# Performance work log

Hardware: AMD Instinct MI355X
Metric: run time of the kernel (lower is better)

The kernel has to match this reference:

```python
import jax, jax.numpy as jnp
import numpy as np

N, E, G = 50000, 800000, 16
H, C = 4, 64  # heads, per-head channels
NEG_SLOPE = 0.2

def gat_conv(x, src, dst, W, att_s, att_d, bias, heads, out_c, concat):
    # x: [N, Fin]; W: [Fin, heads*out_c]; att_s/att_d: [heads, out_c]
    h = (x @ W).reshape(N, heads, out_c)
    a_s = (h * att_s).sum(-1)              # [N, heads]
    a_d = (h * att_d).sum(-1)
    e = a_s[src] + a_d[dst]                # [E, heads]
    e = jnp.where(e >= 0, e, NEG_SLOPE * e)  # leaky_relu
    m = jax.ops.segment_max(e, dst, num_segments=N)
    ex = jnp.exp(e - m[dst])
    den = jax.ops.segment_sum(ex, dst, num_segments=N)
    alpha = ex / (den[dst] + 1e-16)        # segment softmax over incoming edges
    msg = h[src] * alpha[:, :, None]       # [E, heads, out_c]
    out = jax.ops.segment_sum(msg, dst, num_segments=N)
    out = out.reshape(N, heads * out_c) if concat else out.mean(axis=1)
    return out + bias

def setup_inputs() -> dict:
    key = jax.random.key(0)
    ks = jax.random.split(key, 30)
    def g(k, shape, scale=0.05):
        return (jax.random.normal(k, shape, dtype=jnp.float32) * scale)
    inp = {}
    inp['x'] = jax.random.normal(ks[0], (N, 32), dtype=jnp.float32)
    inp['edge_index'] = jax.random.randint(ks[1], (2, E), 0, N, dtype=jnp.int32)
    inp['batch'] = jnp.sort(jax.random.randint(ks[2], (N,), 0, G, dtype=jnp.int32))
    inp['global_features'] = jax.random.normal(ks[3], (G, 4), dtype=jnp.float32)
    # node encoder
    inp['W_enc'] = g(ks[4], (32, C)); inp['b_enc'] = g(ks[5], (C,))
    # conv1: 64 -> 4x64 concat
    inp['W1'] = g(ks[6], (C, H * C)); inp['as1'] = g(ks[7], (H, C)); inp['ad1'] = g(ks[8], (H, C)); inp['b1'] = g(ks[9], (H * C,))
    # conv2: 256 -> 4x64 concat
    inp['W2'] = g(ks[10], (H * C, H * C)); inp['as2'] = g(ks[11], (H, C)); inp['ad2'] = g(ks[12], (H, C)); inp['b2'] = g(ks[13], (H * C,))
    # conv3: 256 -> 1x64 no concat
    inp['W3'] = g(ks[14], (H * C, C)); inp['as3'] = g(ks[15], (1, C)); inp['ad3'] = g(ks[16], (1, C)); inp['b3'] = g(ks[17], (C,))
    # global processor
    inp['Wg'] = g(ks[18], (4, C)); inp['bg'] = g(ks[19], (C,))
    # decoder
    inp['Wd1'] = g(ks[20], (2 * C, C)); inp['bd1'] = g(ks[21], (C,))
    inp['gamma'] = jnp.ones((C,), jnp.float32); inp['beta'] = jnp.zeros((C,), jnp.float32)
    inp['Wd2'] = g(ks[22], (C, 256)); inp['bd2'] = g(ks[23], (256,))
    return inp

def reference(x, edge_index, batch, global_features, W_enc, b_enc,
              W1, as1, ad1, b1, W2, as2, ad2, b2, W3, as3, ad3, b3,
              Wg, bg, Wd1, bd1, gamma, beta, Wd2, bd2):
    # add self-loops (PyG GATConv default)
    loops = jnp.arange(N, dtype=edge_index.dtype)
    src = jnp.concatenate([edge_index[0], loops])
    dst = jnp.concatenate([edge_index[1], loops])
    h = x @ W_enc + b_enc
    h = gat_conv(h, src, dst, W1, as1, ad1, b1, H, C, True)
    h = jax.nn.elu(h)  # dropout is identity in eval
    h = gat_conv(h, src, dst, W2, as2, ad2, b2, H, C, True)
    h = jax.nn.elu(h)
    h = gat_conv(h, src, dst, W3, as3, ad3, b3, 1, C, False)
    # global mean pool per graph
    sums = jax.ops.segment_sum(h, batch, num_segments=G)
    cnts = jax.ops.segment_sum(jnp.ones((N, 1), h.dtype), batch, num_segments=G)
    pooled = sums / jnp.maximum(cnts, 1.0)
    genc = jax.nn.relu(global_features @ Wg + bg)
    z = jnp.concatenate([pooled, genc], axis=1)
    z = z @ Wd1 + bd1
    z = z * gamma + beta  # BatchNorm1d in eval mode (running stats 0/1)
    z = jax.nn.relu(z)
    out = z @ Wd2 + bd2
    return jax.nn.softmax(out, axis=1)
```

## Files before the change

kernel.cpp:

```cpp
#include <hip/hip_runtime.h>
#include <math.h>

#define NEG_SLOPE 0.2f
#define LOG2E 1.4426950408889634f

typedef __attribute__((ext_vector_type(8))) short short8;
typedef __attribute__((ext_vector_type(4))) float f32x4;

__device__ inline float b2f_lo(unsigned int u) {
    union { unsigned int i; float f; } x; x.i = u << 16; return x.f;
}
__device__ inline float b2f_hi(unsigned int u) {
    union { unsigned int i; float f; } x; x.i = u & 0xFFFF0000u; return x.f;
}
__device__ inline unsigned short f2b(float f) {
    union { float f; unsigned int i; } u; u.f = f;
    unsigned int r = u.i + 0x7FFF + ((u.i >> 16) & 1);
    return (unsigned short)(r >> 16);
}

__global__ void prep_kernel(const float* __restrict__ W_enc, const float* __restrict__ b_enc,
                            const float* __restrict__ W1, const float* __restrict__ W2,
                            const float* __restrict__ W3, const float* __restrict__ as1,
                            const float* __restrict__ ad1, const float* __restrict__ b1,
                            unsigned short* __restrict__ Wc1t, float* __restrict__ bc1,
                            unsigned short* __restrict__ Wt2, unsigned short* __restrict__ Wt3,
                            float* __restrict__ u1s, float* __restrict__ u1d,
                            int* __restrict__ counts, float* __restrict__ pooledP,
                            float* __restrict__ cntP, int N, int G, int zc) {
    const int b = blockIdx.x;
    const int t = threadIdx.x;
    if (b < 32) {
        int i = b * 256 + t;
        int h = i >> 11, rem = i & 2047, o = rem >> 5, j = rem & 31;
        float s = 0.0f;
        for (int k = 0; k < 64; k++)
            s += W_enc[j * 64 + k] * W1[k * 256 + h * 64 + o];
        Wc1t[i] = f2b(s);
    } else if (b == 32) {
        float s = b1[t];
        for (int k = 0; k < 64; k++) s += b_enc[k] * W1[k * 256 + t];
        bc1[t] = s;
    } else if (b == 33) {
        int k = t >> 2, h = t & 3;
        float s = 0.0f, d = 0.0f;
        for (int c = 0; c < 64; c++) {
            float w = W1[k * 256 + h * 64 + c];
            s += w * as1[h * 64 + c];
            d += w * ad1[h * 64 + c];
        }
        u1s[k * 4 + h] = s;
        u1d[k * 4 + h] = d;
    } else if (b < 34 + 256) {
        int i = (b - 34) * 256 + t;
        int k = i >> 8, m = i & 255;
        Wt2[(size_t)m * 256 + k] = f2b(W2[i]);
    } else if (b < 34 + 256 + 64) {
        int i = (b - 290) * 256 + t;
        int k = i >> 6, m = i & 63;
        Wt3[(size_t)m * 256 + k] = f2b(W3[i]);
    } else if (b < 354 + zc) {
        int i = (b - 354) * 256 + t;
        if (i < N) counts[i] = 0;
    } else {
        int i = (b - 354 - zc) * 256 + t;
        if (i < 64 * G * 64) pooledP[i] = 0.0f;
        if (i < 64 * G) cntP[i] = 0.0f;
    }
}

__global__ __launch_bounds__(256) void score_x(
        const float* __restrict__ x, const float* __restrict__ W_enc,
        const float* __restrict__ b_enc,
        const float* __restrict__ u1s, const float* __restrict__ u1d,
        unsigned short* __restrict__ x16, float* __restrict__ a_s,
        float* __restrict__ a_d, int N) {
    __shared__ float sUs[32][4], sUd[32][4], sC[8];
    __shared__ float sX[32][33];
    const int t = threadIdx.x;
    if (t < 128) {
        int j = t >> 2, h = t & 3;
        float s = 0.0f, d = 0.0f;
        for (int k = 0; k < 64; k++) {
            float w = W_enc[j * 64 + k];
            s += w * u1s[k * 4 + h];
            d += w * u1d[k * 4 + h];
        }
        sUs[j][h] = s; sUd[j][h] = d;
    } else if (t < 136) {
        int hh = t - 128;
        const float* u = (hh < 4) ? u1s : u1d;
        int h = hh & 3;
        float c = 0.0f;
        for (int k = 0; k < 64; k++) c += b_enc[k] * u[k * 4 + h];
        sC[hh] = c;
    }
    const int n0 = blockIdx.x * 32;
    const int row = t >> 3, col = (t & 7) << 2;
    float4 xv = {0, 0, 0, 0};
    if (n0 + row < N) xv = *(const float4*)&x[(size_t)(n0 + row) * 32 + col];
    sX[row][col + 0] = xv.x; sX[row][col + 1] = xv.y;
    sX[row][col + 2] = xv.z; sX[row][col + 3] = xv.w;
    __syncthreads();
    const int ni = t >> 3, oi = t & 7, h = oi & 3;
    const bool isS = oi < 4;
    float acc = sC[oi];
    #pragma unroll 8
    for (int j = 0; j < 32; j++) acc += sX[ni][j] * (isS ? sUs[j][h] : sUd[j][h]);
    if (n0 + ni < N) {
        float* out = isS ? a_s : a_d;
        out[(size_t)(n0 + ni) * 4 + h] = acc * LOG2E;
    }
    if (n0 + row < N) {
        ushort4 o = {f2b(xv.x), f2b(xv.y), f2b(xv.z), f2b(xv.w)};
        *(ushort4*)&x16[(size_t)(n0 + row) * 32 + col] = o;
    }
}

template<int CPW, int SCORES>
__global__ __launch_bounds__(256) void gemm_mfma(const unsigned short* __restrict__ A16,
                                                 const unsigned short* __restrict__ Bt16,
                                                 unsigned short* __restrict__ C16,
                                                 const float* __restrict__ att_s,
                                                 const float* __restrict__ att_d,
                                                 float* __restrict__ a_s,
                                                 float* __restrict__ a_d,
                                                 int Nrows, int K, int M, int H) {
    constexpr int BN = CPW * 64;
    __shared__ unsigned short sA[64][40];
    __shared__ unsigned short sB[BN][40];
    const int tid = threadIdx.x;
    const int wave = tid >> 6;
    const int lane = tid & 63;
    const int quad = lane >> 4;
    const int l16 = lane & 15;
    const int row0 = blockIdx.x * 64;
    const int col0 = blockIdx.y * BN;
    const int sr = tid >> 2;
    const int sk = (tid & 3) << 3;

    f32x4 acc[4][CPW];
    #pragma unroll
    for (int i = 0; i < 4; i++)
        #pragma unroll
        for (int j = 0; j < CPW; j++) acc[i][j] = (f32x4){0,0,0,0};

    for (int kt = 0; kt < K; kt += 32) {
        __syncthreads();
        {
            int r = row0 + sr;
            uint4 z = {0,0,0,0};
            *(uint4*)&sA[sr][sk] = (r < Nrows) ? *(const uint4*)&A16[(size_t)r * K + kt + sk] : z;
        }
        #pragma unroll
        for (int i = 0; i < CPW; i++) {
            int c = col0 + sr + i * 64;
            *(uint4*)&sB[sr + i * 64][sk] = *(const uint4*)&Bt16[(size_t)c * K + kt + sk];
        }
        __syncthreads();
        short8 bf[CPW];
        #pragma unroll
        for (int j = 0; j < CPW; j++)
            bf[j] = *(const short8*)&sB[wave * (CPW * 16) + j * 16 + l16][quad * 8];
        #pragma unroll
        for (int i = 0; i < 4; i++) {
            short8 af = *(const short8*)&sA[i * 16 + l16][quad * 8];
            #pragma unroll
            for (int j = 0; j < CPW; j++)
                acc[i][j] = __builtin_amdgcn_mfma_f32_16x16x32_bf16(af, bf[j], acc[i][j], 0, 0, 0);
        }
    }
    if (SCORES) {
        __shared__ float sSD[64][CPW][2];
        for (int t = tid; t < 64 * CPW * 2; t += 256) ((float*)sSD)[t] = 0.0f;
        __syncthreads();
        const int hib = (wave * CPW * 16) >> 6;
        float avs[CPW], avd[CPW];
        #pragma unroll
        for (int j = 0; j < CPW; j++) {
            int c = col0 + wave * (CPW * 16) + j * 16 + l16;
            avs[j] = att_s[c];
            avd[j] = att_d[c];
        }
        #pragma unroll
        for (int i = 0; i < 4; i++) {
            float ps[4] = {0,0,0,0}, pd[4] = {0,0,0,0};
            #pragma unroll
            for (int j = 0; j < CPW; j++)
                #pragma unroll
                for (int r = 0; r < 4; r++) {
                    ps[r] += acc[i][j][r] * avs[j];
                    pd[r] += acc[i][j][r] * avd[j];
                }
            #pragma unroll
            for (int off = 1; off < 16; off <<= 1)
                #pragma unroll
                for (int r = 0; r < 4; r++) {
                    ps[r] += __shfl_xor(ps[r], off);
                    pd[r] += __shfl_xor(pd[r], off);
                }
            if (l16 == 0) {
                #pragma unroll
                for (int r = 0; r < 4; r++) {
                    atomicAdd(&sSD[i * 16 + quad * 4 + r][hib][0], ps[r]);
                    atomicAdd(&sSD[i * 16 + quad * 4 + r][hib][1], pd[r]);
                }
            }
        }
        __syncthreads();
        for (int t = tid; t < 64 * CPW; t += 256) {
            int row = t & 63, hb = t >> 6;
            int r = row0 + row;
            if (r < Nrows) {
                int hg = (col0 >> 6) + hb;
                a_s[r * H + hg] = sSD[row][hb][0] * LOG2E;
                a_d[r * H + hg] = sSD[row][hb][1] * LOG2E;
            }
        }
    }
    #pragma unroll
    for (int i = 0; i < 4; i++) {
        #pragma unroll
        for (int j = 0; j < CPW; j++) {
            int col = col0 + wave * (CPW * 16) + j * 16 + l16;
            #pragma unroll
            for (int r = 0; r < 4; r++) {
                int row = row0 + i * 16 + quad * 4 + r;
                if (row < Nrows) C16[(size_t)row * M + col] = f2b(acc[i][j][r]);
            }
        }
    }
}

__global__ __launch_bounds__(256) void gemm_bd32(const unsigned short* __restrict__ A16,
                                                 const unsigned short* __restrict__ Bt16,
                                                 const float* __restrict__ bias,
                                                 unsigned short* __restrict__ C16,
                                                 int Nrows) {
    __shared__ unsigned short sA[64][40];
    __shared__ unsigned short sB[64][40];
    const int tid = threadIdx.x;
    const int wave = tid >> 6;
    const int lane = tid & 63;
    const int quad = lane >> 4;
    const int l16 = lane & 15;
    const int h = blockIdx.y;
    const int row0 = blockIdx.x * 64;
    const int sr = tid >> 2;
    const int sk = (tid & 3) << 3;

    {
        int r = row0 + sr;
        uint4 z = {0,0,0,0};
        *(uint4*)&sA[sr][sk] = (r < Nrows)
            ? *(const uint4*)&A16[(size_t)r * 128 + h * 32 + sk] : z;
        *(uint4*)&sB[sr][sk] = *(const uint4*)&Bt16[(size_t)(h * 64 + sr) * 32 + sk];
    }
    __syncthreads();
    short8 bf = *(const short8*)&sB[wave * 16 + l16][quad * 8];
    f32x4 acc[4];
    #pragma unroll
    for (int i = 0; i < 4; i++) {
        short8 af = *(const short8*)&sA[i * 16 + l16][quad * 8];
        acc[i] = __builtin_amdgcn_mfma_f32_16x16x32_bf16(af, bf, (f32x4){0,0,0,0}, 0, 0, 0);
    }
    const int col = h * 64 + wave * 16 + l16;
    const float bb = bias[col];
    #pragma unroll
    for (int i = 0; i < 4; i++) {
        #pragma unroll
        for (int r = 0; r < 4; r++) {
            int row = row0 + i * 16 + quad * 4 + r;
            if (row < Nrows) {
                float v = acc[i][r] + bb;
                v = (v > 0.0f) ? v : expm1f(v);
                C16[(size_t)row * 256 + col] = f2b(v);
            }
        }
    }
}

__global__ void edge_hist_kernel(const int* __restrict__ ei, int* __restrict__ counts,
                                 int E, int Et) {
    int e = blockIdx.x * 256 + threadIdx.x;
    if (e >= Et) return;
    int d = (e < E) ? ei[E + e] : e - E;
    atomicAdd(&counts[d], 1);
}

__global__ __launch_bounds__(1024) void scan_blocks(int* __restrict__ counts,
                                                    int* __restrict__ blockSums, int N) {
    __shared__ int wsum[16];
    const int tid = threadIdx.x;
    const int lane = tid & 63;
    const int wave = tid >> 6;
    int i = blockIdx.x * 1024 + tid;
    int v = (i < N) ? counts[i] : 0;
    int s = v;
    #pragma unroll
    for (int off = 1; off < 64; off <<= 1) {
        int t = __shfl_up(s, off);
        if (lane >= off) s += t;
    }
    if (lane == 63) wsum[wave] = s;
    __syncthreads();
    if (wave == 0 && lane < 16) {
        int ws = wsum[lane];
        #pragma unroll
        for (int off = 1; off < 16; off <<= 1) {
            int t = __shfl_up(ws, off);
            if (lane >= off) ws += t;
        }
        wsum[lane] = ws;
    }
    __syncthreads();
    int waveOff = (wave > 0) ? wsum[wave - 1] : 0;
    int incl = s + waveOff;
    if (i < N) counts[i] = incl - v;
    if (tid == 1023) blockSums[blockIdx.x] = incl;
}

__global__ void scan_add2(const int* __restrict__ excl, const int* __restrict__ blockSums,
                          int nb, int* __restrict__ offsets, int* __restrict__ cursor,
                          int N, int Et) {
    __shared__ int sbs[64];
    if (threadIdx.x < 64) {
        int lane = threadIdx.x;
        int v = (lane < nb) ? blockSums[lane] : 0;
        int s = v;
        #pragma unroll
        for (int off = 1; off < 64; off <<= 1) {
            int t = __shfl_up(s, off);
            if (lane >= off) s += t;
        }
        sbs[lane] = s - v;
    }
    __syncthreads();
    int i = blockIdx.x * 256 + threadIdx.x;
    if (i < N) {
        int o = excl[i] + sbs[i >> 10];
        offsets[i] = o;
        cursor[i] = o;
    }
    if (i == N) offsets[N] = Et;
}

__global__ void edge_sort_kernel(const int* __restrict__ ei, int* __restrict__ cursor,
                                 int* __restrict__ srcS, int E, int Et) {
    int e = blockIdx.x * 256 + threadIdx.x;
    if (e >= Et) return;
    int s, d;
    if (e < E) { s = ei[e]; d = ei[E + e]; } else { s = d = e - E; }
    int pos = atomicAdd(&cursor[d], 1);
    srcS[pos] = s;
}

__global__ __launch_bounds__(256) void gat_agg_x32(
        const int* __restrict__ offsets, const int* __restrict__ srcS,
        const float4* __restrict__ a_s4, const float4* __restrict__ a_d4,
        const unsigned short* __restrict__ x16,
        unsigned short* __restrict__ aggX,
        int N) {
    __shared__ float4 wlds[4][64];
    __shared__ int slds[4][64];
    const int wid = threadIdx.x >> 6;
    const int n = blockIdx.x * 4 + wid;
    if (n >= N) return;
    const int lane = threadIdx.x & 63;
    const int q = lane >> 4;
    const int l16 = lane & 15;
    const int start = offsets[n], end = offsets[n + 1];
    const float4 ad = a_d4[n];
    float2 acc0 = {0,0}, acc1 = {0,0}, acc2 = {0,0}, acc3 = {0,0};
    float4 den = {0,0,0,0};
    const int loff = l16 << 1;

    for (int e0 = start; e0 < end; e0 += 64) {
        const int cnt = min(64, end - e0);
        if (lane < cnt) {
            int sB = srcS[e0 + lane];
            slds[wid][lane] = sB;
            const float4 as = a_s4[sB];
            float x0 = as.x + ad.x; x0 = fmaxf(x0, NEG_SLOPE * x0);
            float x1 = as.y + ad.y; x1 = fmaxf(x1, NEG_SLOPE * x1);
            float x2 = as.z + ad.z; x2 = fmaxf(x2, NEG_SLOPE * x2);
            float x3 = as.w + ad.w; x3 = fmaxf(x3, NEG_SLOPE * x3);
            wlds[wid][lane] = (float4){exp2f(x0), exp2f(x1), exp2f(x2), exp2f(x3)};
        }
        int j = q;
        for (; j + 12 < cnt; j += 16) {
            int ss[4]; float4 ww[4]; unsigned int gg[4];
            #pragma unroll
            for (int u = 0; u < 4; u++) {
                ss[u] = slds[wid][j + 4 * u];
                ww[u] = wlds[wid][j + 4 * u];
            }
            #pragma unroll
            for (int u = 0; u < 4; u++)
                gg[u] = *(const unsigned int*)&x16[((size_t)ss[u] << 5) + loff];
            #pragma unroll
            for (int u = 0; u < 4; u++) {
                const float vl = b2f_lo(gg[u]), vh = b2f_hi(gg[u]);
                acc0.x += ww[u].x * vl; acc0.y += ww[u].x * vh;
                acc1.x += ww[u].y * vl; acc1.y += ww[u].y * vh;
                acc2.x += ww[u].z * vl; acc2.y += ww[u].z * vh;
                acc3.x += ww[u].w * vl; acc3.y += ww[u].w * vh;
                den.x += ww[u].x; den.y += ww[u].y; den.z += ww[u].z; den.w += ww[u].w;
            }
        }
        for (; j + 4 < cnt; j += 8) {
            const int s0 = slds[wid][j], s1 = slds[wid][j + 4];
            const float4 w0 = wlds[wid][j], w1 = wlds[wid][j + 4];
            const unsigned int g0 = *(const unsigned int*)&x16[((size_t)s0 << 5) + loff];
            const unsigned int g1 = *(const unsigned int*)&x16[((size_t)s1 << 5) + loff];
            const float vl0 = b2f_lo(g0), vh0 = b2f_hi(g0);
            const float vl1 = b2f_lo(g1), vh1 = b2f_hi(g1);
            acc0.x += w0.x * vl0 + w1.x * vl1; acc0.y += w0.x * vh0 + w1.x * vh1;
            acc1.x += w0.y * vl0 + w1.y * vl1; acc1.y += w0.y * vh0 + w1.y * vh1;
            acc2.x += w0.z * vl0 + w1.z * vl1; acc2.y += w0.z * vh0 + w1.z * vh1;
            acc3.x += w0.w * vl0 + w1.w * vl1; acc3.y += w0.w * vh0 + w1.w * vh1;
            den.x += w0.x + w1.x; den.y += w0.y + w1.y;
            den.z += w0.z + w1.z; den.w += w0.w + w1.w;
        }
        for (; j < cnt; j += 4) {
            const int s = slds[wid][j];
            const float4 w = wlds[wid][j];
            const unsigned int g = *(const unsigned int*)&x16[((size_t)s << 5) + loff];
            const float vl = b2f_lo(g), vh = b2f_hi(g);
            acc0.x += w.x * vl; acc0.y += w.x * vh;
            acc1.x += w.y * vl; acc1.y += w.y * vh;
            acc2.x += w.z * vl; acc2.y += w.z * vh;
            acc3.x += w.w * vl; acc3.y += w.w * vh;
            den.x += w.x; den.y += w.y; den.z += w.z; den.w += w.w;
        }
    }
    #pragma unroll
    for (int off = 16; off < 64; off <<= 1) {
        acc0.x += __shfl_xor(acc0.x, off); acc0.y += __shfl_xor(acc0.y, off);
        acc1.x += __shfl_xor(acc1.x, off); acc1.y += __shfl_xor(acc1.y, off);
        acc2.x += __shfl_xor(acc2.x, off); acc2.y += __shfl_xor(acc2.y, off);
        acc3.x += __shfl_xor(acc3.x, off); acc3.y += __shfl_xor(acc3.y, off);
        den.x += __shfl_xor(den.x, off); den.y += __shfl_xor(den.y, off);
        den.z += __shfl_xor(den.z, off); den.w += __shfl_xor(den.w, off);
    }
    if (q == 0) {
        const float i0 = 1.0f / (den.x + 1e-16f);
        const float i1 = 1.0f / (den.y + 1e-16f);
        const float i2 = 1.0f / (den.z + 1e-16f);
        const float i3 = 1.0f / (den.w + 1e-16f);
        unsigned int o0 = (unsigned int)f2b(acc0.x * i0) | ((unsigned int)f2b(acc0.y * i0) << 16);
        unsigned int o1 = (unsigned int)f2b(acc1.x * i1) | ((unsigned int)f2b(acc1.y * i1) << 16);
        unsigned int o2 = (unsigned int)f2b(acc2.x * i2) | ((unsigned int)f2b(acc2.y * i2) << 16);
        unsigned int o3 = (unsigned int)f2b(acc3.x * i3) | ((unsigned int)f2b(acc3.y * i3) << 16);
        *(unsigned int*)&aggX[((size_t)n << 7) + 0 * 32 + loff] = o0;
        *(unsigned int*)&aggX[((size_t)n << 7) + 1 * 32 + loff] = o1;
        *(unsigned int*)&aggX[((size_t)n << 7) + 2 * 32 + loff] = o2;
        *(unsigned int*)&aggX[((size_t)n << 7) + 3 * 32 + loff] = o3;
    }
}

__global__ __launch_bounds__(256) void gat_fused4(
        const int* __restrict__ offsets, const int* __restrict__ srcS,
        const float4* __restrict__ a_s4, const float4* __restrict__ a_d4,
        const unsigned short* __restrict__ hW16, const float* __restrict__ bias,
        unsigned short* __restrict__ out16, int N) {
    __shared__ float wlds[4][64][4];
    __shared__ int slds[4][64];
    const int wid = threadIdx.x >> 6;
    const int n = blockIdx.x * 4 + wid;
    if (n >= N) return;
    const int lane = threadIdx.x & 63;
    const int quad = lane >> 4;
    const int start = offsets[n], end = offsets[n + 1];
    const float4 ad = a_d4[n];
    float4 acc = {0, 0, 0, 0};
    float den = 0.0f;
    const int loff = lane << 2;

    for (int e0 = start; e0 < end; e0 += 64) {
        const int cnt = min(64, end - e0);
        if (lane < cnt) {
            int sB = srcS[e0 + lane];
            slds[wid][lane] = sB;
            const float4 as = a_s4[sB];
            float x0 = as.x + ad.x; x0 = fmaxf(x0, NEG_SLOPE * x0);
            float x1 = as.y + ad.y; x1 = fmaxf(x1, NEG_SLOPE * x1);
            float x2 = as.z + ad.z; x2 = fmaxf(x2, NEG_SLOPE * x2);
            float x3 = as.w + ad.w; x3 = fmaxf(x3, NEG_SLOPE * x3);
            wlds[wid][lane][0] = exp2f(x0);
            wlds[wid][lane][1] = exp2f(x1);
            wlds[wid][lane][2] = exp2f(x2);
            wlds[wid][lane][3] = exp2f(x3);
        }
        int j = 0;
        for (; j + 4 <= cnt; j += 4) {
            const int s0 = __builtin_amdgcn_readfirstlane(slds[wid][j + 0]);
            const int s1 = __builtin_amdgcn_readfirstlane(slds[wid][j + 1]);
            const int s2 = __builtin_amdgcn_readfirstlane(slds[wid][j + 2]);
            const int s3 = __builtin_amdgcn_readfirstlane(slds[wid][j + 3]);
            const float w0 = wlds[wid][j + 0][quad];
            const float w1 = wlds[wid][j + 1][quad];
            const float w2 = wlds[wid][j + 2][quad];
            const float w3 = wlds[wid][j + 3][quad];
            const uint2 h0 = *(const uint2*)&hW16[((size_t)s0 << 8) + loff];
            const uint2 h1 = *(const uint2*)&hW16[((size_t)s1 << 8) + loff];
            const uint2 h2 = *(const uint2*)&hW16[((size_t)s2 << 8) + loff];
            const uint2 h3 = *(const uint2*)&hW16[((size_t)s3 << 8) + loff];
            acc.x += w0 * b2f_lo(h0.x); acc.y += w0 * b2f_hi(h0.x);
            acc.z += w0 * b2f_lo(h0.y); acc.w += w0 * b2f_hi(h0.y);
            acc.x += w1 * b2f_lo(h1.x); acc.y += w1 * b2f_hi(h1.x);
            acc.z += w1 * b2f_lo(h1.y); acc.w += w1 * b2f_hi(h1.y);
            acc.x += w2 * b2f_lo(h2.x); acc.y += w2 * b2f_hi(h2.x);
            acc.z += w2 * b2f_lo(h2.y); acc.w += w2 * b2f_hi(h2.y);
            acc.x += w3 * b2f_lo(h3.x); acc.y += w3 * b2f_hi(h3.x);
            acc.z += w3 * b2f_lo(h3.y); acc.w += w3 * b2f_hi(h3.y);
            den += (w0 + w1) + (w2 + w3);
        }
        for (; j < cnt; j++) {
            const int s = __builtin_amdgcn_readfirstlane(slds[wid][j]);
            const float w = wlds[wid][j][quad];
            const uint2 hv = *(const uint2*)&hW16[((size_t)s << 8) + loff];
            acc.x += w * b2f_lo(hv.x); acc.y += w * b2f_hi(hv.x);
            acc.z += w * b2f_lo(hv.y); acc.w += w * b2f_hi(hv.y);
            den += w;
        }
    }

    const float inv = 1.0f / (den + 1e-16f);
    const float4 bb = *(const float4*)&bias[loff];
    float v0 = acc.x * inv + bb.x; v0 = (v0 > 0.0f) ? v0 : expm1f(v0);
    float v1 = acc.y * inv + bb.y; v1 = (v1 > 0.0f) ? v1 : expm1f(v1);
    float v2 = acc.z * inv + bb.z; v2 = (v2 > 0.0f) ? v2 : expm1f(v2);
    float v3 = acc.w * inv + bb.w; v3 = (v3 > 0.0f) ? v3 : expm1f(v3);
    uint2 o;
    o.x = (unsigned int)f2b(v0) | ((unsigned int)f2b(v1) << 16);
    o.y = (unsigned int)f2b(v2) | ((unsigned int)f2b(v3) << 16);
    *(uint2*)&out16[(size_t)n * 256 + loff] = o;
}

__global__ __launch_bounds__(256) void gat_fused1(
        const int* __restrict__ offsets, const int* __restrict__ srcS,
        const float* __restrict__ a_s, const float* __restrict__ a_d,
        const unsigned short* __restrict__ hW16, const float* __restrict__ bias,
        const int* __restrict__ batch,
        float* __restrict__ pooledP, float* __restrict__ cntP, int N, int G) {
    __shared__ float wlds[4][64];
    __shared__ int slds[4][64];
    __shared__ float2 sOut[4][32];
    __shared__ int sG[4];
    const int wid = threadIdx.x >> 6;
    const int n = blockIdx.x * 4 + wid;
    const bool valid = n < N;
    const int lane = threadIdx.x & 63;
    const int half = lane >> 5;
    const int l32 = lane & 31;
    const int start = valid ? offsets[n] : 0;
    const int end   = valid ? offsets[n + 1] : 0;
    const float ad  = valid ? a_d[n] : 0.0f;
    float accx = 0.0f, accy = 0.0f, den = 0.0f;
    const int loff = l32 << 1;

    for (int e0 = start; e0 < end; e0 += 64) {
        const int cnt_ = min(64, end - e0);
        if (lane < cnt_) {
            int sB = srcS[e0 + lane];
            slds[wid][lane] = sB;
            float ev = a_s[sB] + ad;
            ev = fmaxf(ev, NEG_SLOPE * ev);
            wlds[wid][lane] = exp2f(ev);
        }
        int j = half;
        for (; j + 8 <= cnt_ + half; j += 8) {
            const int s0 = slds[wid][j + 0];
            const int s1 = slds[wid][j + 2];
            const int s2 = slds[wid][j + 4];
            const int s3 = slds[wid][j + 6];
            const float w0 = wlds[wid][j + 0];
            const float w1 = wlds[wid][j + 2];
            const float w2 = wlds[wid][j + 4];
            const float w3 = wlds[wid][j + 6];
            const unsigned int h0 = *(const unsigned int*)&hW16[((size_t)s0 << 6) + loff];
            const unsigned int h1 = *(const unsigned int*)&hW16[((size_t)s1 << 6) + loff];
            const unsigned int h2 = *(const unsigned int*)&hW16[((size_t)s2 << 6) + loff];
            const unsigned int h3 = *(const unsigned int*)&hW16[((size_t)s3 << 6) + loff];
            accx += w0 * b2f_lo(h0); accy += w0 * b2f_hi(h0);
            accx += w1 * b2f_lo(h1); accy += w1 * b2f_hi(h1);
            accx += w2 * b2f_lo(h2); accy += w2 * b2f_hi(h2);
            accx += w3 * b2f_lo(h3); accy += w3 * b2f_hi(h3);
            den += (w0 + w1) + (w2 + w3);
        }
        for (; j < cnt_; j += 2) {
            const int s = slds[wid][j];
            const float w = wlds[wid][j];
            const unsigned int hv = *(const unsigned int*)&hW16[((size_t)s << 6) + loff];
            accx += w * b2f_lo(hv);
            accy += w * b2f_hi(hv);
            den += w;
        }
    }
    accx += __shfl_xor(accx, 32);
    accy += __shfl_xor(accy, 32);
    den  += __shfl_xor(den, 32);
    if (half == 0) {
        if (valid) {
            const float inv = 1.0f / (den + 1e-16f);
            sOut[wid][l32] = (float2){accx * inv + bias[loff], accy * inv + bias[loff + 1]};
        } else {
            sOut[wid][l32] = (float2){0.0f, 0.0f};
        }
        if (l32 == 0) sG[wid] = valid ? batch[n] : -1;
    }
    __syncthreads();
    const int p = blockIdx.x & 63;
    if (wid == 0 && half == 0) {
        const int g0 = sG[0], g1 = sG[1], g2 = sG[2], g3 = sG[3];
        if (g0 >= 0 && g1 == g0 && g2 == g0 && g3 == g0) {
            const float2 s0 = sOut[0][l32], s1 = sOut[1][l32];
            const float2 s2 = sOut[2][l32], s3 = sOut[3][l32];
            float* base = pooledP + ((size_t)p * G + g0) * 64;
            atomicAdd(&base[loff],     (s0.x + s1.x) + (s2.x + s3.x));
            atomicAdd(&base[loff + 1], (s0.y + s1.y) + (s2.y + s3.y));
            if (l32 == 0) atomicAdd(&cntP[p * G + g0], 4.0f);
        } else {
            #pragma unroll
            for (int w = 0; w < 4; w++) {
                const int g = sG[w];
                if (g >= 0) {
                    const float2 s = sOut[w][l32];
                    float* base = pooledP + ((size_t)p * G + g) * 64;
                    atomicAdd(&base[loff], s.x);
                    atomicAdd(&base[loff + 1], s.y);
                    if (l32 == 0) atomicAdd(&cntP[p * G + g], 1.0f);
                }
            }
        }
    }
}

__global__ __launch_bounds__(256) void final_kernel(
        const float* __restrict__ pooledP, const float* __restrict__ cntP,
        const float* __restrict__ gf, const float* __restrict__ Wg,
        const float* __restrict__ bg, const float* __restrict__ Wd1,
        const float* __restrict__ bd1, const float* __restrict__ gamma,
        const float* __restrict__ beta, const float* __restrict__ Wd2,
        const float* __restrict__ bd2, float* __restrict__ out, int G) {
    const int g = blockIdx.x;
    const int tid = threadIdx.x;
    const int lane = tid & 63;
    const int wave = tid >> 6;
    __shared__ float sPart[4][64];
    __shared__ float sCntTot;
    __shared__ float spg[128];
    __shared__ float sz[64];
    __shared__ float wred[8];

    {
        const int c = lane;
        const int pg = wave;
        float a = 0.0f;
        #pragma unroll
        for (int p = 0; p < 16; p++)
            a += pooledP[((size_t)(pg * 16 + p) * G + g) * 64 + c];
        sPart[pg][c] = a;
        if (pg == 1) {
            float cv = cntP[c * G + g];
            #pragma unroll
            for (int off = 32; off > 0; off >>= 1) cv += __shfl_xor(cv, off);
            if (c == 0) sCntTot = cv;
        }
    }
    __syncthreads();
    if (tid < 64) {
        spg[tid] = (sPart[0][tid] + sPart[1][tid] + sPart[2][tid] + sPart[3][tid])
                   / fmaxf(sCntTot, 1.0f);
    } else if (tid < 128) {
        int c = tid - 64;
        float v = bg[c];
        #pragma unroll
        for (int k = 0; k < 4; k++) v += gf[g * 4 + k] * Wg[k * 64 + c];
        spg[64 + c] = fmaxf(v, 0.0f);
    }
    __syncthreads();
    if (tid < 64) {
        float v = bd1[tid];
        #pragma unroll 8
        for (int k = 0; k < 128; k++) v += spg[k] * Wd1[k * 64 + tid];
        v = v * gamma[tid] + beta[tid];
        sz[tid] = fmaxf(v, 0.0f);
    }
    __syncthreads();
    float v = bd2[tid];
    #pragma unroll 8
    for (int k = 0; k < 64; k++) v += sz[k] * Wd2[k * 256 + tid];
    float m = v;
    #pragma unroll
    for (int off = 32; off > 0; off >>= 1) m = fmaxf(m, __shfl_xor(m, off));
    if (lane == 0) wred[wave] = m;
    __syncthreads();
    float M = fmaxf(fmaxf(wred[0], wred[1]), fmaxf(wred[2], wred[3]));
    float e = expf(v - M);
    float s = e;
    #pragma unroll
    for (int off = 32; off > 0; off >>= 1) s += __shfl_xor(s, off);
    if (lane == 0) wred[4 + wave] = s;
    __syncthreads();
    float S = (wred[4] + wred[5]) + (wred[6] + wred[7]);
    out[g * 256 + tid] = e / S;
}

extern "C" void kernel_launch(void* const* d_in, const int* in_sizes, int n_in,
                              void* d_out, int out_size, void* d_ws, size_t ws_size,
                              hipStream_t stream) {
    const float* x     = (const float*)d_in[0];
    const int*   ei    = (const int*)  d_in[1];
    const int*   batch = (const int*)  d_in[2];
    const float* gf    = (const float*)d_in[3];
    const float* W_enc = (const float*)d_in[4];
    const float* b_enc = (const float*)d_in[5];
    const float* W1  = (const float*)d_in[6];
    const float* as1 = (const float*)d_in[7];
    const float* ad1 = (const float*)d_in[8];
    const float* b1  = (const float*)d_in[9];
    const float* W2  = (const float*)d_in[10];
    const float* as2 = (const float*)d_in[11];
    const float* ad2 = (const float*)d_in[12];
    const float* b2  = (const float*)d_in[13];
    const float* W3  = (const float*)d_in[14];
    const float* as3 = (const float*)d_in[15];
    const float* ad3 = (const float*)d_in[16];
    const float* b3  = (const float*)d_in[17];
    const float* Wg  = (const float*)d_in[18];
    const float* bg  = (const float*)d_in[19];
    const float* Wd1 = (const float*)d_in[20];
    const float* bd1 = (const float*)d_in[21];
    const float* gm  = (const float*)d_in[22];
    const float* bt  = (const float*)d_in[23];
    const float* Wd2 = (const float*)d_in[24];
    const float* bd2 = (const float*)d_in[25];

    const int N  = in_sizes[2];
    const int E  = in_sizes[1] / 2;
    const int G  = in_sizes[3] / 4;
    const int Et = E + N;

    unsigned short* h16a = (unsigned short*)d_ws;
    unsigned short* h16b = h16a + (size_t)N * 256;
    unsigned short* h1_16 = h16b + (size_t)N * 256;
    unsigned short* x16  = h1_16 + (size_t)N * 64;
    unsigned short* Wc1t = x16 + (size_t)N * 32;
    unsigned short* Wt2  = Wc1t + 4 * 64 * 32;
    unsigned short* Wt3  = Wt2 + 256 * 256;
    float* bc1    = (float*)(Wt3 + 64 * 256);
    float* a_s    = bc1 + 256;
    float* a_d    = a_s + (size_t)N * 4;
    float* u1s    = a_d + (size_t)N * 4;
    float* u1d    = u1s + 256;
    float* pooledP = u1d + 256;
    float* cntP   = pooledP + (size_t)64 * G * 64;
    int*   offsets = (int*)(cntP + 64 * G);
    int*   srcS    = offsets + (N + 1);
    int*   counts  = srcS + Et;
    int*   cursor  = counts + N;
    int*   blockSums = cursor + N;

    dim3 blk(256);
    auto cdiv = [](int a, int b) { return (a + b - 1) / b; };
    const int eBlocks = cdiv(Et, 256);
    const int rowBlocks = cdiv(N, 64);
    const int nScanBlocks = cdiv(N, 1024);
    const int zc = cdiv(N, 256);
    const int z2 = cdiv(64 * G * 64, 256);

    prep_kernel<<<354 + zc + z2, blk, 0, stream>>>(W_enc, b_enc, W1, W2, W3, as1, ad1, b1,
                                                   Wc1t, bc1, Wt2, Wt3, u1s, u1d,
                                                   counts, pooledP, cntP, N, G, zc);
    edge_hist_kernel<<<eBlocks, blk, 0, stream>>>(ei, counts, E, Et);
    scan_blocks<<<nScanBlocks, 1024, 0, stream>>>(counts, blockSums, N);
    scan_add2<<<cdiv(N + 1, 256), blk, 0, stream>>>(counts, blockSums, nScanBlocks,
                                                    offsets, cursor, N, Et);
    edge_sort_kernel<<<eBlocks, blk, 0, stream>>>(ei, cursor, srcS, E, Et);

    score_x<<<cdiv(N, 32), blk, 0, stream>>>(x, W_enc, b_enc, u1s, u1d, x16, a_s, a_d, N);

    gat_agg_x32<<<cdiv(N, 4), blk, 0, stream>>>(offsets, srcS, (const float4*)a_s,
                                                (const float4*)a_d, x16, h16a, N);
    gemm_bd32<<<dim3(rowBlocks, 4), blk, 0, stream>>>(h16a, Wc1t, bc1, h16b, N);

    gemm_mfma<2, 1><<<dim3(rowBlocks, 2), blk, 0, stream>>>(h16b, Wt2, h16a,
                                                            as2, ad2, a_s, a_d, N, 256, 256, 4);
    gat_fused4<<<cdiv(N, 4), blk, 0, stream>>>(offsets, srcS, (const float4*)a_s,
                                               (const float4*)a_d, h16a, b2, h16b, N);

    gemm_mfma<1, 1><<<dim3(rowBlocks, 1), blk, 0, stream>>>(h16b, Wt3, h1_16,
                                                            as3, ad3, a_s, a_d, N, 256, 64, 1);
    gat_fused1<<<cdiv(N, 4), blk, 0, stream>>>(offsets, srcS, a_s, a_d, h1_16, b3,
                                               batch, pooledP, cntP, N, G);

    final_kernel<<<G, blk, 0, stream>>>(pooledP, cntP, gf, Wg, bg, Wd1, bd1, gm, bt, Wd2, bd2,
                                        (float*)d_out, G);
}
```

Measured before the change: 424.6 us.

## Fuse conv1 output GEMM into conv2 GEMM and precompute conv3 attention scores

Merges the per-head conv1 projection (bias plus ELU) with the conv2 weight GEMM into one kernel. The 64x256 intermediate tile now stays in LDS and is never written to or reread from global memory. Conv3 attention logits are computed inside gat_fused4 by dotting the ELU output with W3·att vectors precomputed in prep, so the conv3 GEMM drops its score epilogue. In exchange the fused kernel uses about 54KB of LDS and launches one block per row tile instead of 2D grids, which lowers occupancy and parallelism. The conv3 scores come from fp32 activations rather than the bf16-rounded GEMM output, so they differ slightly numerically.

```diff
diff --git a/kernel.cpp b/kernel.cpp
--- a/kernel.cpp
+++ b/kernel.cpp
@@ -23,9 +23,11 @@
                             const float* __restrict__ W1, const float* __restrict__ W2,
                             const float* __restrict__ W3, const float* __restrict__ as1,
                             const float* __restrict__ ad1, const float* __restrict__ b1,
+                            const float* __restrict__ as3, const float* __restrict__ ad3,
                             unsigned short* __restrict__ Wc1t, float* __restrict__ bc1,
                             unsigned short* __restrict__ Wt2, unsigned short* __restrict__ Wt3,
                             float* __restrict__ u1s, float* __restrict__ u1d,
+                            float* __restrict__ u3s, float* __restrict__ u3d,
                             int* __restrict__ counts, float* __restrict__ pooledP,
                             float* __restrict__ cntP, int N, int G, int zc) {
     const int b = blockIdx.x;
@@ -51,19 +53,27 @@
         }
         u1s[k * 4 + h] = s;
         u1d[k * 4 + h] = d;
-    } else if (b < 34 + 256) {
-        int i = (b - 34) * 256 + t;
+    } else if (b == 34) {
+        float s = 0.0f, d = 0.0f;
+        for (int o = 0; o < 64; o++) {
+            float w = W3[t * 64 + o];
+            s += w * as3[o];
+            d += w * ad3[o];
+        }
+        u3s[t] = s; u3d[t] = d;
+    } else if (b < 35 + 256) {
+        int i = (b - 35) * 256 + t;
         int k = i >> 8, m = i & 255;
         Wt2[(size_t)m * 256 + k] = f2b(W2[i]);
-    } else if (b < 34 + 256 + 64) {
-        int i = (b - 290) * 256 + t;
+    } else if (b < 35 + 256 + 64) {
+        int i = (b - 291) * 256 + t;
         int k = i >> 6, m = i & 63;
         Wt3[(size_t)m * 256 + k] = f2b(W3[i]);
-    } else if (b < 354 + zc) {
-        int i = (b - 354) * 256 + t;
+    } else if (b < 355 + zc) {
+        int i = (b - 355) * 256 + t;
         if (i < N) counts[i] = 0;
     } else {
-        int i = (b - 354 - zc) * 256 + t;
+        int i = (b - 355 - zc) * 256 + t;
         if (i < 64 * G * 64) pooledP[i] = 0.0f;
         if (i < 64 * G) cntP[i] = 0.0f;
     }
@@ -232,49 +242,136 @@
     }
 }
 
-__global__ __launch_bounds__(256) void gemm_bd32(const unsigned short* __restrict__ A16,
-                                                 const unsigned short* __restrict__ Bt16,
-                                                 const float* __restrict__ bias,
-                                                 unsigned short* __restrict__ C16,
-                                                 int Nrows) {
-    __shared__ unsigned short sA[64][40];
-    __shared__ unsigned short sB[64][40];
+__global__ __launch_bounds__(256) void gemm_c12(
+        const unsigned short* __restrict__ aggX,
+        const unsigned short* __restrict__ Wc1t,
+        const float* __restrict__ bc1,
+        const unsigned short* __restrict__ Wt2,
+        const float* __restrict__ att_s,
+        const float* __restrict__ att_d,
+        float* __restrict__ a_s, float* __restrict__ a_d,
+        unsigned short* __restrict__ C16,
+        int Nrows) {
+    __shared__ unsigned short sH[64][264];
+    __shared__ unsigned short sB[256][40];
+    __shared__ float sSD[64][4][2];
     const int tid = threadIdx.x;
     const int wave = tid >> 6;
     const int lane = tid & 63;
     const int quad = lane >> 4;
     const int l16 = lane & 15;
-    const int h = blockIdx.y;
     const int row0 = blockIdx.x * 64;
     const int sr = tid >> 2;
     const int sk = (tid & 3) << 3;
 
+    #pragma unroll
+    for (int h = 0; h < 4; h++) {
+        __syncthreads();
+        {
+            int r = row0 + sr;
+            uint4 z = {0,0,0,0};
+            *(uint4*)&sB[sr][sk] = (r < Nrows)
+                ? *(const uint4*)&aggX[(size_t)r * 128 + h * 32 + sk] : z;
+            *(uint4*)&sB[64 + sr][sk] = *(const uint4*)&Wc1t[(size_t)(h * 64 + sr) * 32 + sk];
+        }
+        __syncthreads();
+        short8 bf = *(const short8*)&sB[64 + wave * 16 + l16][quad * 8];
+        const int col = h * 64 + wave * 16 + l16;
+        const float bb = bc1[col];
+        #pragma unroll
+        for (int i = 0; i < 4; i++) {
+            short8 af = *(const short8*)&sB[i * 16 + l16][quad * 8];
+            f32x4 acc = __builtin_amdgcn_mfma_f32_16x16x32_bf16(af, bf, (f32x4){0,0,0,0}, 0, 0, 0);
+            #pragma unroll
+            for (int r = 0; r < 4; r++) {
+                float v = acc[r] + bb;
+                v = (v > 0.0f) ? v : expm1f(v);
+                sH[i * 16 + quad * 4 + r][col] = f2b(v);
+            }
+        }
+    }
+
+    f32x4 acc2[4][4];
+    #pragma unroll
+    for (int i = 0; i < 4; i++)
+        #pragma unroll
+        for (int j = 0; j < 4; j++) acc2[i][j] = (f32x4){0,0,0,0};
+
+    for (int kt = 0; kt < 256; kt += 32) {
+        __syncthreads();
+        #pragma unroll
+        for (int i = 0; i < 4; i++) {
+            int c = sr + i * 64;
+            *(uint4*)&sB[c][sk] = *(const uint4*)&Wt2[(size_t)c * 256 + kt + sk];
+        }
+        __syncthreads();
+        short8 bf2[4];
+        #pragma unroll
+        for (int j = 0; j < 4; j++)
+            bf2[j] = *(const short8*)&sB[wave * 64 + j * 16 + l16][quad * 8];
+        #pragma unroll
+        for (int i = 0; i < 4; i++) {
+            short8 af = *(const short8*)&sH[i * 16 + l16][kt + quad * 8];
+            #pragma unroll
+            for (int j = 0; j < 4; j++)
+                acc2[i][j] = __builtin_amdgcn_mfma_f32_16x16x32_bf16(af, bf2[j], acc2[i][j], 0, 0, 0);
+        }
+    }
+
     {
-        int r = row0 + sr;
-        uint4 z = {0,0,0,0};
-        *(uint4*)&sA[sr][sk] = (r < Nrows)
-            ? *(const uint4*)&A16[(size_t)r * 128 + h * 32 + sk] : z;
-        *(uint4*)&sB[sr][sk] = *(const uint4*)&Bt16[(size_t)(h * 64 + sr) * 32 + sk];
-    }
-    __syncthreads();
-    short8 bf = *(const short8*)&sB[wave * 16 + l16][quad * 8];
-    f32x4 acc[4];
+        for (int t = tid; t < 512; t += 256) ((float*)sSD)[t] = 0.0f;
+        __syncthreads();
+        float avs[4], avd[4];
+        #pragma unroll
+        for (int j = 0; j < 4; j++) {
+            int c = wave * 64 + j * 16 + l16;
+            avs[j] = att_s[c];
+            avd[j] = att_d[c];
+        }
+        #pragma unroll
+        for (int i = 0; i < 4; i++) {
+            float ps[4] = {0,0,0,0}, pd[4] = {0,0,0,0};
+            #pragma unroll
+            for (int j = 0; j < 4; j++)
+                #pragma unroll
+                for (int r = 0; r < 4; r++) {
+                    ps[r] += acc2[i][j][r] * avs[j];
+                    pd[r] += acc2[i][j][r] * avd[j];
+                }
+            #pragma unroll
+            for (int off = 1; off < 16; off <<= 1)
+                #pragma unroll
+                for (int r = 0; r < 4; r++) {
+                    ps[r] += __shfl_xor(ps[r], off);
+                    pd[r] += __shfl_xor(pd[r], off);
+                }
+            if (l16 == 0) {
+                #pragma unroll
+                for (int r = 0; r < 4; r++) {
+                    atomicAdd(&sSD[i * 16 + quad * 4 + r][wave][0], ps[r]);
+                    atomicAdd(&sSD[i * 16 + quad * 4 + r][wave][1], pd[r]);
+                }
+            }
+        }
+        __syncthreads();
+        {
+            int row = tid & 63, hb = tid >> 6;
+            int r = row0 + row;
+            if (r < Nrows) {
+                a_s[r * 4 + hb] = sSD[row][hb][0] * LOG2E;
+                a_d[r * 4 + hb] = sSD[row][hb][1] * LOG2E;
+            }
+        }
+    }
     #pragma unroll
     for (int i = 0; i < 4; i++) {
-        short8 af = *(const short8*)&sA[i * 16 + l16][quad * 8];
-        acc[i] = __builtin_amdgcn_mfma_f32_16x16x32_bf16(af, bf, (f32x4){0,0,0,0}, 0, 0, 0);
-    }
-    const int col = h * 64 + wave * 16 + l16;
-    const float bb = bias[col];
-    #pragma unroll
-    for (int i = 0; i < 4; i++) {
-        #pragma unroll
-        for (int r = 0; r < 4; r++) {
-            int row = row0 + i * 16 + quad * 4 + r;
-            if (row < Nrows) {
-                float v = acc[i][r] + bb;
-                v = (v > 0.0f) ? v : expm1f(v);
-                C16[(size_t)row * 256 + col] = f2b(v);
+        #pragma unroll
+        for (int j = 0; j < 4; j++) {
+            int col = wave * 64 + j * 16 + l16;
+            #pragma unroll
+            for (int r = 0; r < 4; r++) {
+                int row = row0 + i * 16 + quad * 4 + r;
+                if (row < Nrows) C16[(size_t)row * 256 + col] = f2b(acc2[i][j][r]);
             }
         }
     }
@@ -463,6 +560,8 @@
         const int* __restrict__ offsets, const int* __restrict__ srcS,
         const float4* __restrict__ a_s4, const float4* __restrict__ a_d4,
         const unsigned short* __restrict__ hW16, const float* __restrict__ bias,
+        const float* __restrict__ u3s, const float* __restrict__ u3d,
+        float* __restrict__ a_s3, float* __restrict__ a_d3,
         unsigned short* __restrict__ out16, int N) {
     __shared__ float wlds[4][64][4];
     __shared__ int slds[4][64];
@@ -532,6 +631,21 @@
     float v1 = acc.y * inv + bb.y; v1 = (v1 > 0.0f) ? v1 : expm1f(v1);
     float v2 = acc.z * inv + bb.z; v2 = (v2 > 0.0f) ? v2 : expm1f(v2);
     float v3 = acc.w * inv + bb.w; v3 = (v3 > 0.0f) ? v3 : expm1f(v3);
+    {
+        const float4 us = *(const float4*)&u3s[loff];
+        const float4 ud = *(const float4*)&u3d[loff];
+        float ps = v0 * us.x + v1 * us.y + v2 * us.z + v3 * us.w;
+        float pd = v0 * ud.x + v1 * ud.y + v2 * ud.z + v3 * ud.w;
+        #pragma unroll
+        for (int off = 1; off < 64; off <<= 1) {
+            ps += __shfl_xor(ps, off);
+            pd += __shfl_xor(pd, off);
+        }
+        if (lane == 0) {
+            a_s3[n] = ps * LOG2E;
+            a_d3[n] = pd * LOG2E;
+        }
+    }
     uint2 o;
     o.x = (unsigned int)f2b(v0) | ((unsigned int)f2b(v1) << 16);
     o.y = (unsigned int)f2b(v2) | ((unsigned int)f2b(v3) << 16);
@@ -753,9 +867,13 @@
     float* bc1    = (float*)(Wt3 + 64 * 256);
     float* a_s    = bc1 + 256;
     float* a_d    = a_s + (size_t)N * 4;
-    float* u1s    = a_d + (size_t)N * 4;
+    float* a_s3   = a_d + (size_t)N * 4;
+    float* a_d3   = a_s3 + N;
+    float* u1s    = a_d3 + N;
     float* u1d    = u1s + 256;
-    float* pooledP = u1d + 256;
+    float* u3s    = u1d + 256;
+    float* u3d    = u3s + 256;
+    float* pooledP = u3d + 256;
     float* cntP   = pooledP + (size_t)64 * G * 64;
     int*   offsets = (int*)(cntP + 64 * G);
     int*   srcS    = offsets + (N + 1);
@@ -771,8 +889,9 @@
     const int zc = cdiv(N, 256);
     const int z2 = cdiv(64 * G * 64, 256);
 
-    prep_kernel<<<354 + zc + z2, blk, 0, stream>>>(W_enc, b_enc, W1, W2, W3, as1, ad1, b1,
-                                                   Wc1t, bc1, Wt2, Wt3, u1s, u1d,
+    prep_kernel<<<355 + zc + z2, blk, 0, stream>>>(W_enc, b_enc, W1, W2, W3, as1, ad1, b1,
+                                                   as3, ad3, Wc1t, bc1, Wt2, Wt3,
+                                                   u1s, u1d, u3s, u3d,
                                                    counts, pooledP, cntP, N, G, zc);
     edge_hist_kernel<<<eBlocks, blk, 0, stream>>>(ei, counts, E, Et);
     scan_blocks<<<nScanBlocks, 1024, 0, stream>>>(counts, blockSums, N);
@@ -783,17 +902,18 @@
     score_x<<<cdiv(N, 32), blk, 0, stream>>>(x, W_enc, b_enc, u1s, u1d, x16, a_s, a_d, N);
 
     gat_agg_x32<<<cdiv(N, 4), blk, 0, stream>>>(offsets, srcS, (const float4*)a_s,
-                                                (const float4*)a_d, x16, h16a, N);
-    gemm_bd32<<<dim3(rowBlocks, 4), blk, 0, stream>>>(h16a, Wc1t, bc1, h16b, N);
-
-    gemm_mfma<2, 1><<<dim3(rowBlocks, 2), blk, 0, stream>>>(h16b, Wt2, h16a,
-                                                            as2, ad2, a_s, a_d, N, 256, 256, 4);
+                                                (const float4*)a_d, x16, h16b, N);
+    gemm_c12<<<rowBlocks, blk, 0, stream>>>(h16b, Wc1t, bc1, Wt2, as2, ad2,
+                                            a_s, a_d, h16a, N);
+
     gat_fused4<<<cdiv(N, 4), blk, 0, stream>>>(offsets, srcS, (const float4*)a_s,
-                                               (const float4*)a_d, h16a, b2, h16b, N);
-
-    gemm_mfma<1, 1><<<dim3(rowBlocks, 1), blk, 0, stream>>>(h16b, Wt3, h1_16,
-                                                            as3, ad3, a_s, a_d, N, 256, 64, 1);
-    gat_fused1<<<cdiv(N, 4), blk, 0, stream>>>(offsets, srcS, a_s, a_d, h1_16, b3,
+                                               (const float4*)a_d, h16a, b2,
+                                               u3s, u3d, a_s3, a_d3, h16b, N);
+
+    gemm_mfma<1, 0><<<dim3(rowBlocks, 1), blk, 0, stream>>>(h16b, Wt3, h1_16,
+                                                            nullptr, nullptr, nullptr, nullptr,
+                                                            N, 256, 64, 1);
+    gat_fused1<<<cdiv(N, 4), blk, 0, stream>>>(offsets, srcS, a_s3, a_d3, h1_16, b3,
                                                batch, pooledP, cntP, N, G);
 
     final_kernel<<<G, blk, 0, stream>>>(pooledP, cntP, gf, Wg, bg, Wd1, bd1, gm, bt, Wd2, bd2,
```

Measured after the change: 404.6 us. 1.05x faster.
